# Performance work log

Hardware: AMD Instinct MI355X
Metric: run time of the kernel (lower is better)

Reference implementation:

```python
import jax, jax.numpy as jnp
import numpy as np

N_HEADS = 32
N_KV_HEADS = 8
HEAD_DIM = 128  # hidden 4096 / 32
NEG_INF = -1e9


def _apply_rope(x, cos, sin):
    # x: [B, S, H, D]; cos/sin: [S, D//2] -> complex multiply on (even, odd) pairs
    B, S, H, D = x.shape
    xr = x.reshape(B, S, H, D // 2, 2)
    a, b = xr[..., 0], xr[..., 1]
    c = cos[None, :, None, :]
    s = sin[None, :, None, :]
    out = jnp.stack([a * c - b * s, a * s + b * c], axis=-1)
    return out.reshape(B, S, H, D)


def setup_inputs() -> dict:
    key = jax.random.key(0)
    ks = jax.random.split(key, 8)
    B, S, HID = 1, 2048, 4096
    hidden_states = jax.random.normal(ks[0], (B, S, HID), dtype=jnp.float32)
    # causal additive mask [1,1,S,S]
    causal = jnp.tril(jnp.ones((S, S), dtype=bool))
    attention_mask = jnp.where(causal, 0.0, NEG_INF).astype(jnp.float32)[None, None]
    # true rotary frequencies (theta=500000 as in llama3)
    half = HEAD_DIM // 2
    inv_freq = 1.0 / (500000.0 ** (np.arange(0, half, dtype=np.float32) / half))
    angles = np.arange(S, dtype=np.float32)[:, None] * inv_freq[None, :]
    freqs_cos = jnp.asarray(np.cos(angles), dtype=jnp.float32)
    freqs_sin = jnp.asarray(np.sin(angles), dtype=jnp.float32)
    sc = 0.02
    wq = jax.random.normal(ks[1], (HID, HID), dtype=jnp.float32) * sc
    wk = jax.random.normal(ks[2], (N_KV_HEADS * HEAD_DIM, HID), dtype=jnp.float32) * sc
    wv = jax.random.normal(ks[3], (N_KV_HEADS * HEAD_DIM, HID), dtype=jnp.float32) * sc
    wo = jax.random.normal(ks[4], (HID, HID), dtype=jnp.float32) * sc
    return {"hidden_states": hidden_states, "attention_mask": attention_mask,
            "freqs_cos": freqs_cos, "freqs_sin": freqs_sin,
            "wq": wq, "wk": wk, "wv": wv, "wo": wo}


def reference(hidden_states, attention_mask, freqs_cos, freqs_sin, wq, wk, wv, wo):
    B, S, HID = hidden_states.shape
    n_rep = N_HEADS // N_KV_HEADS
    # projections (torch Linear: x @ W.T)
    q = (hidden_states @ wq.T).reshape(B, S, N_HEADS, HEAD_DIM)
    k = (hidden_states @ wk.T).reshape(B, S, N_KV_HEADS, HEAD_DIM)
    v = (hidden_states @ wv.T).reshape(B, S, N_KV_HEADS, HEAD_DIM)
    # rotary on q (full cos/sin) and k
    q = _apply_rope(q, freqs_cos, freqs_sin)
    k = _apply_rope(k, freqs_cos, freqs_sin)
    # [B, H, S, D]
    q = q.transpose(0, 2, 1, 3)
    k = k.transpose(0, 2, 1, 3)
    v = v.transpose(0, 2, 1, 3)
    # GQA: repeat_interleave kv heads
    k = jnp.repeat(k, n_rep, axis=1)
    v = jnp.repeat(v, n_rep, axis=1)
    scores = jnp.einsum("bhqd,bhkd->bhqk", q, k) / jnp.sqrt(jnp.float32(HEAD_DIM))
    scores = scores + attention_mask
    probs = jax.nn.softmax(scores.astype(jnp.float32), axis=-1)
    attn = jnp.einsum("bhqk,bhkd->bhqd", probs, v)
    attn = attn.transpose(0, 2, 1, 3).reshape(B, S, N_HEADS * HEAD_DIM)
    return attn @ wo.T
```

## Files before the change

### kernel.cpp

```cpp
#include <hip/hip_runtime.h>
#include <hip/hip_bf16.h>
#include <math.h>

#define SEQ 2048
#define HID 4096
#define NH 32
#define NKV 8
#define HD 128
#define KVG (NH / NKV)
#define NQKV 6144

typedef __bf16 bf16x8 __attribute__((ext_vector_type(8)));
typedef float  f32x4  __attribute__((ext_vector_type(4)));

__device__ __forceinline__ unsigned short f2bf(float f) {
  union { float f; unsigned int u; } v; v.f = f;
  unsigned int r = v.u + 0x7FFFu + ((v.u >> 16) & 1u);
  return (unsigned short)(r >> 16);
}
__device__ __forceinline__ float bf2f(unsigned short h) {
  union { unsigned int u; float f; } v; v.u = ((unsigned int)h) << 16;
  return v.f;
}

__device__ __forceinline__ void glds16(const unsigned short* g, unsigned short* l) {
  __builtin_amdgcn_global_load_lds(
      (const __attribute__((address_space(1))) void*)g,
      (__attribute__((address_space(3))) void*)l, 16, 0, 0);
}

#define MFMA_BF16 __builtin_amdgcn_mfma_f32_16x16x32_bf16

__global__ __launch_bounds__(256) void cvt_all(
    const float* __restrict__ H, const float* __restrict__ wq,
    const float* __restrict__ wk, const float* __restrict__ wv,
    const float* __restrict__ wo, unsigned short* __restrict__ ws)
{
  const long G1 = 1l << 20;
  const long M1 = 1l << 20;
  long g = (long)blockIdx.x * 256 + threadIdx.x;
  const float* src; unsigned short* dst; long rel;
  if      (g < 2 * G1) { src = H;  dst = ws;           rel = g;          }
  else if (g < 6 * G1) { src = wq; dst = ws + 8 * M1;  rel = g - 2 * G1; }
  else if (g < 7 * G1) { src = wk; dst = ws + 24 * M1; rel = g - 6 * G1; }
  else if (g < 8 * G1) { src = wv; dst = ws + 28 * M1; rel = g - 7 * G1; }
  else                 { src = wo; dst = ws + 32 * M1; rel = g - 8 * G1; }
  float4 v = ((const float4*)src)[rel];
  ushort4 o;
  o.x = f2bf(v.x); o.y = f2bf(v.y); o.z = f2bf(v.z); o.w = f2bf(v.w);
  ((ushort4*)dst)[rel] = o;
}

template<bool F32OUT>
__global__ __launch_bounds__(256) void gemm_nt(
    const unsigned short* __restrict__ A,
    const unsigned short* __restrict__ B,
    void* __restrict__ Cv,
    int M, int N, int K)
{
  __shared__ unsigned short As[128 * 64];
  __shared__ unsigned short Bs[128 * 64];
  const int t = threadIdx.x;
  const int lane = t & 63, wid = t >> 6;
  const int quad = lane >> 4, l16 = lane & 15;
  const int wm = (wid & 1) * 64, wn = (wid >> 1) * 64;
  const int m0 = blockIdx.y * 128, n0 = blockIdx.x * 128;

  int srow[4], sgch[4];
  const unsigned short* ga[4];
  const unsigned short* gb[4];
  unsigned short* la[4];
  unsigned short* lb[4];
  #pragma unroll
  for (int j = 0; j < 4; j++) {
    int pj = (wid * 4 + j) * 64 + lane;
    srow[j] = pj >> 3;
    sgch[j] = (pj & 7) ^ (srow[j] & 7);
    ga[j] = A + (size_t)(m0 + srow[j]) * K + sgch[j] * 8;
    gb[j] = B + (size_t)(n0 + srow[j]) * K + sgch[j] * 8;
    la[j] = &As[(wid * 4 + j) * 512];
    lb[j] = &Bs[(wid * 4 + j) * 512];
  }

  const f32x4 fzero = {0.f, 0.f, 0.f, 0.f};
  f32x4 acc[4][4];
  #pragma unroll
  for (int i = 0; i < 4; i++)
    #pragma unroll
    for (int j = 0; j < 4; j++) acc[i][j] = fzero;

  for (int k0 = 0; k0 < K; k0 += 64) {
    __syncthreads();
    #pragma unroll
    for (int j = 0; j < 4; j++) {
      glds16(ga[j], la[j]);
      glds16(gb[j], lb[j]);
      ga[j] += 64; gb[j] += 64;
    }
    __syncthreads();

    #pragma unroll
    for (int ks = 0; ks < 2; ks++) {
      bf16x8 af[4], bfr[4];
      #pragma unroll
      for (int mt = 0; mt < 4; mt++) {
        int row = wm + mt * 16 + l16;
        int cp = (ks * 4 + quad) ^ (l16 & 7);
        af[mt] = *(const bf16x8*)(&As[(row * 8 + cp) * 8]);
      }
      #pragma unroll
      for (int nt = 0; nt < 4; nt++) {
        int row = wn + nt * 16 + l16;
        int cp = (ks * 4 + quad) ^ (l16 & 7);
        bfr[nt] = *(const bf16x8*)(&Bs[(row * 8 + cp) * 8]);
      }
      #pragma unroll
      for (int mt = 0; mt < 4; mt++)
        #pragma unroll
        for (int nt = 0; nt < 4; nt++)
          acc[mt][nt] = MFMA_BF16(af[mt], bfr[nt], acc[mt][nt], 0, 0, 0);
    }
  }

  #pragma unroll
  for (int mt = 0; mt < 4; mt++)
    #pragma unroll
    for (int nt = 0; nt < 4; nt++)
      #pragma unroll
      for (int r = 0; r < 4; r++) {
        int row = m0 + wm + mt * 16 + quad * 4 + r;
        int col = n0 + wn + nt * 16 + l16;
        float v = acc[mt][nt][r];
        if (F32OUT) ((float*)Cv)[(size_t)row * N + col] = v;
        else        ((unsigned short*)Cv)[(size_t)row * N + col] = f2bf(v);
      }
}

__global__ __launch_bounds__(256) void rope_vtrans(
    const unsigned short* __restrict__ QKVr,
    const float* __restrict__ cosT,
    const float* __restrict__ sinT,
    unsigned short* __restrict__ Qh,
    unsigned short* __restrict__ Kh,
    unsigned short* __restrict__ Vtg)
{
  __shared__ unsigned short T[64 * 66];
  int hh = blockIdx.y;
  int bx = blockIdx.x;
  int t = threadIdx.x;
  if (hh < NH + NKV) {
    int sub = t >> 6, d2 = t & 63;
    int s = bx * 4 + sub;
    float c = cosT[s * 64 + d2], sn = sinT[s * 64 + d2];
    if (hh < NH) {
      const unsigned short* src = QKVr + (size_t)s * NQKV + hh * HD;
      unsigned short* dst = Qh + ((size_t)hh * SEQ + s) * HD;
      float a = bf2f(src[2 * d2]), b = bf2f(src[2 * d2 + 1]);
      dst[2 * d2]     = f2bf(a * c - b * sn);
      dst[2 * d2 + 1] = f2bf(a * sn + b * c);
    } else {
      int h = hh - NH;
      const unsigned short* src = QKVr + (size_t)s * NQKV + HID + h * HD;
      unsigned short* dst = Kh + ((size_t)h * SEQ + s) * HD;
      float a = bf2f(src[2 * d2]), b = bf2f(src[2 * d2 + 1]);
      dst[2 * d2]     = f2bf(a * c - b * sn);
      dst[2 * d2 + 1] = f2bf(a * sn + b * c);
    }
  } else {
    int idx = bx >> 5;
    int kvh = idx >> 1, d0 = (idx & 1) * 64;
    int s0 = (bx & 31) * 64;
    int si = t >> 2, dchunk = t & 3;
    const unsigned short* src = QKVr + (size_t)(s0 + si) * NQKV + HID + NKV * HD + kvh * HD + d0 + dchunk * 16;
    uint4 a = *(const uint4*)src;
    uint4 b = *(const uint4*)(src + 8);
    unsigned int va[8] = {a.x, a.y, a.z, a.w, b.x, b.y, b.z, b.w};
    #pragma unroll
    for (int j = 0; j < 8; j++)
      *(unsigned int*)(&T[si * 66 + dchunk * 16 + j * 2]) = va[j];
    __syncthreads();
    int di = t >> 2, schunk = t & 3;
    unsigned short px[16];
    #pragma unroll
    for (int j = 0; j < 16; j++) px[j] = T[(schunk * 16 + j) * 66 + di];
    unsigned short* dst = Vtg + ((size_t)kvh * HD + d0 + di) * SEQ + s0 + schunk * 16;
    *(uint4*)dst = *(uint4*)px;
    *(uint4*)(dst + 8) = *(uint4*)(px + 8);
  }
}

__global__ __launch_bounds__(256) void flash_kernel(
    const unsigned short* __restrict__ Qh,
    const unsigned short* __restrict__ Kh,
    const unsigned short* __restrict__ Vtg,
    unsigned short* __restrict__ Obf)
{
  __shared__ unsigned short Ks[2][64 * 128];
  __shared__ unsigned short Vs[2][128 * 64];
  __shared__ unsigned short Ps[4][16 * 72];

  const int h = blockIdx.y;
  const int pairp = blockIdx.x;
  const int kvh = h / KVG;
  const int t = threadIdx.x;
  const int lane = t & 63, w = t >> 6;
  const int quad = lane >> 4, l16 = lane & 15;
  const float scale = 0.08838834764831845f;
  const float SHIFT = 8.0f;

  bf16x8 ones;
  #pragma unroll
  for (int j = 0; j < 8; j++) ones[j] = (__bf16)1.0f;

  int krow[4], kgch[4], vrow[4], vgch[4];
  #pragma unroll
  for (int j = 0; j < 4; j++) {
    int pj = (w * 4 + j) * 64 + lane;
    krow[j] = pj >> 4; kgch[j] = (pj & 15) ^ (krow[j] & 15);
    vrow[j] = pj >> 3; vgch[j] = (pj & 7) ^ (vrow[j] & 7);
  }

  const unsigned short* Kbase = Kh + (size_t)kvh * SEQ * HD;
  const unsigned short* Vbase = Vtg + (size_t)kvh * HD * SEQ;

  auto stage = [&](int buf, int kv0) {
    #pragma unroll
    for (int j = 0; j < 4; j++) {
      glds16(Kbase + (size_t)(kv0 + krow[j]) * HD + kgch[j] * 8,
             &Ks[buf][(w * 4 + j) * 512]);
      glds16(Vbase + (size_t)vrow[j] * SEQ + kv0 + vgch[j] * 8,
             &Vs[buf][(w * 4 + j) * 512]);
    }
  };

  unsigned short* Pw = Ps[w];
  const f32x4 fzero = {0.f, 0.f, 0.f, 0.f};

  #pragma unroll
  for (int pass = 0; pass < 2; pass++) {
    const int qt = pass ? (31 - pairp) : pairp;
    const int q0 = qt * 64;
    const int q = q0 + w * 16 + l16;

    bf16x8 aq[4];
    const unsigned short* Qp = Qh + ((size_t)h * SEQ + q0 + w * 16 + l16) * HD;
    #pragma unroll
    for (int ks = 0; ks < 4; ks++) aq[ks] = *(const bf16x8*)(Qp + ks * 32 + quad * 8);

    f32x4 o[8];
    #pragma unroll
    for (int dt = 0; dt < 8; dt++) o[dt] = fzero;
    f32x4 lacc = fzero;

    const int nIt = (q0 >> 6) + 1;
    stage(0, 0);

    for (int it = 0; it < nIt; it++) {
      const int buf = it & 1;
      const int kv0 = it << 6;
      if (it + 1 < nIt) {
        stage(buf ^ 1, kv0 + 64);
        asm volatile("s_waitcnt vmcnt(8)" ::: "memory");
      } else {
        asm volatile("s_waitcnt vmcnt(0)" ::: "memory");
      }
      __builtin_amdgcn_s_barrier();

      const unsigned short* Kb = Ks[buf];
      const unsigned short* Vb = Vs[buf];

      f32x4 sc[4];
      #pragma unroll
      for (int kvt = 0; kvt < 4; kvt++) sc[kvt] = fzero;
      __builtin_amdgcn_s_setprio(1);
      #pragma unroll
      for (int ks = 0; ks < 4; ks++)
        #pragma unroll
        for (int kvt = 0; kvt < 4; kvt++) {
          int row = kvt * 16 + l16;
          int cp = (ks * 4 + quad) ^ l16;
          bf16x8 bk = *(const bf16x8*)(&Kb[(row * 16 + cp) * 8]);
          sc[kvt] = MFMA_BF16(bk, aq[ks], sc[kvt], 0, 0, 0);
        }
      __builtin_amdgcn_s_setprio(0);

      #pragma unroll
      for (int kvt = 0; kvt < 4; kvt++) {
        unsigned short ph[4];
        #pragma unroll
        for (int r = 0; r < 4; r++) {
          int kv = kv0 + kvt * 16 + quad * 4 + r;
          float p = (kv > q) ? 0.f : __expf(fmaf(sc[kvt][r], scale, -SHIFT));
          ph[r] = f2bf(p);
        }
        *(uint2*)(&Pw[l16 * 72 + kvt * 16 + quad * 4]) = *(const uint2*)ph;
      }

      __builtin_amdgcn_s_setprio(1);
      #pragma unroll
      for (int ks2 = 0; ks2 < 2; ks2++) {
        bf16x8 ap = *(const bf16x8*)(&Pw[l16 * 72 + ks2 * 32 + quad * 8]);
        lacc = MFMA_BF16(ap, ones, lacc, 0, 0, 0);
        #pragma unroll
        for (int dt = 0; dt < 8; dt++) {
          int row = dt * 16 + l16;
          int cp = (ks2 * 4 + quad) ^ (l16 & 7);
          bf16x8 bv = *(const bf16x8*)(&Vb[(row * 8 + cp) * 8]);
          o[dt] = MFMA_BF16(ap, bv, o[dt], 0, 0, 0);
        }
      }
      __builtin_amdgcn_s_setprio(0);
      __builtin_amdgcn_s_barrier();
    }

    #pragma unroll
    for (int dt = 0; dt < 8; dt++)
      #pragma unroll
      for (int r = 0; r < 4; r++) {
        int qq = q0 + w * 16 + quad * 4 + r;
        int d = dt * 16 + l16;
        Obf[(size_t)qq * HID + h * HD + d] = f2bf(o[dt][r] / lacc[r]);
      }
  }
}

extern "C" void kernel_launch(void* const* d_in, const int* in_sizes, int n_in,
                              void* d_out, int out_size, void* d_ws, size_t ws_size,
                              hipStream_t stream) {
  const float* H    = (const float*)d_in[0];
  const float* cosT = (const float*)d_in[2];
  const float* sinT = (const float*)d_in[3];
  const float* wq   = (const float*)d_in[4];
  const float* wk   = (const float*)d_in[5];
  const float* wv   = (const float*)d_in[6];
  const float* wo   = (const float*)d_in[7];

  unsigned short* ws = (unsigned short*)d_ws;
  const size_t M1 = 1u << 20;
  unsigned short* Hb   = ws;
  unsigned short* Wqkv = ws + (size_t)8  * M1;
  unsigned short* Wob  = ws + (size_t)32 * M1;
  unsigned short* QKVr = ws + (size_t)48 * M1;
  unsigned short* Qh   = ws + (size_t)8  * M1;
  unsigned short* Kh   = ws + (size_t)16 * M1;
  unsigned short* Vtg  = ws + (size_t)18 * M1;
  unsigned short* attn = ws;

  cvt_all<<<49152, 256, 0, stream>>>(H, wq, wk, wv, wo, ws);

  gemm_nt<false><<<dim3(48, 16), 256, 0, stream>>>(Hb, Wqkv, QKVr, SEQ, NQKV, HID);

  rope_vtrans<<<dim3(512, NH + NKV + 1), 256, 0, stream>>>(QKVr, cosT, sinT, Qh, Kh, Vtg);

  flash_kernel<<<dim3(16, NH), 256, 0, stream>>>(Qh, Kh, Vtg, attn);

  gemm_nt<true><<<dim3(32, 16), 256, 0, stream>>>(attn, Wob, d_out, SEQ, HID, HID);
}
```

Baseline: 482.5 us.

## Vectorize RoPE, split V transpose, grid-stride convert, skip mask off-diagonal

The fp32-to-bf16 convert kernel becomes a grid-stride loop over 2048 blocks instead of launching one thread per float4. RoPE for Q/K moves to its own kernel, where each thread handles 8 elements with 16-byte loads and stores and vectorized cos/sin reads, and the V transpose gets a separate launch. In flash attention the causal mask compare now runs only on diagonal tiles. Together these cut scalar memory traffic, launch overhead and per-element branching, at the cost of one extra kernel launch.

```diff
diff --git a/kernel.cpp b/kernel.cpp
--- a/kernel.cpp
+++ b/kernel.cpp
@@ -38,17 +38,20 @@
 {
   const long G1 = 1l << 20;
   const long M1 = 1l << 20;
-  long g = (long)blockIdx.x * 256 + threadIdx.x;
-  const float* src; unsigned short* dst; long rel;
-  if      (g < 2 * G1) { src = H;  dst = ws;           rel = g;          }
-  else if (g < 6 * G1) { src = wq; dst = ws + 8 * M1;  rel = g - 2 * G1; }
-  else if (g < 7 * G1) { src = wk; dst = ws + 24 * M1; rel = g - 6 * G1; }
-  else if (g < 8 * G1) { src = wv; dst = ws + 28 * M1; rel = g - 7 * G1; }
-  else                 { src = wo; dst = ws + 32 * M1; rel = g - 8 * G1; }
-  float4 v = ((const float4*)src)[rel];
-  ushort4 o;
-  o.x = f2bf(v.x); o.y = f2bf(v.y); o.z = f2bf(v.z); o.w = f2bf(v.w);
-  ((ushort4*)dst)[rel] = o;
+  const long TOT = 12 * G1;
+  const long stride = (long)gridDim.x * 256;
+  for (long g = (long)blockIdx.x * 256 + threadIdx.x; g < TOT; g += stride) {
+    const float* src; unsigned short* dst; long rel;
+    if      (g < 2 * G1) { src = H;  dst = ws;           rel = g;          }
+    else if (g < 6 * G1) { src = wq; dst = ws + 8 * M1;  rel = g - 2 * G1; }
+    else if (g < 7 * G1) { src = wk; dst = ws + 24 * M1; rel = g - 6 * G1; }
+    else if (g < 8 * G1) { src = wv; dst = ws + 28 * M1; rel = g - 7 * G1; }
+    else                 { src = wo; dst = ws + 32 * M1; rel = g - 8 * G1; }
+    float4 v = ((const float4*)src)[rel];
+    ushort4 o;
+    o.x = f2bf(v.x); o.y = f2bf(v.y); o.z = f2bf(v.z); o.w = f2bf(v.w);
+    ((ushort4*)dst)[rel] = o;
+  }
 }
 
 template<bool F32OUT>
@@ -136,57 +139,71 @@
       }
 }
 
-__global__ __launch_bounds__(256) void rope_vtrans(
+__global__ __launch_bounds__(256) void rope_qk(
     const unsigned short* __restrict__ QKVr,
     const float* __restrict__ cosT,
     const float* __restrict__ sinT,
     unsigned short* __restrict__ Qh,
-    unsigned short* __restrict__ Kh,
+    unsigned short* __restrict__ Kh)
+{
+  const int hh = blockIdx.y;
+  const int c = blockIdx.x * 256 + threadIdx.x;
+  const int s = c >> 4, ch = c & 15;
+  const int d0 = ch * 8;
+
+  const unsigned short* src;
+  unsigned short* dst;
+  if (hh < NH) {
+    src = QKVr + (size_t)s * NQKV + hh * HD + d0;
+    dst = Qh + ((size_t)hh * SEQ + s) * HD + d0;
+  } else {
+    int h = hh - NH;
+    src = QKVr + (size_t)s * NQKV + HID + h * HD + d0;
+    dst = Kh + ((size_t)h * SEQ + s) * HD + d0;
+  }
+
+  float4 cv = *(const float4*)(cosT + s * 64 + (d0 >> 1));
+  float4 sv = *(const float4*)(sinT + s * 64 + (d0 >> 1));
+  float cs[4] = {cv.x, cv.y, cv.z, cv.w};
+  float sn[4] = {sv.x, sv.y, sv.z, sv.w};
+
+  union { uint4 v; unsigned short u[8]; } in, out;
+  in.v = *(const uint4*)src;
+  #pragma unroll
+  for (int j = 0; j < 4; j++) {
+    float a = bf2f(in.u[2 * j]), b = bf2f(in.u[2 * j + 1]);
+    out.u[2 * j]     = f2bf(a * cs[j] - b * sn[j]);
+    out.u[2 * j + 1] = f2bf(a * sn[j] + b * cs[j]);
+  }
+  *(uint4*)dst = out.v;
+}
+
+__global__ __launch_bounds__(256) void vtrans(
+    const unsigned short* __restrict__ QKVr,
     unsigned short* __restrict__ Vtg)
 {
   __shared__ unsigned short T[64 * 66];
-  int hh = blockIdx.y;
   int bx = blockIdx.x;
   int t = threadIdx.x;
-  if (hh < NH + NKV) {
-    int sub = t >> 6, d2 = t & 63;
-    int s = bx * 4 + sub;
-    float c = cosT[s * 64 + d2], sn = sinT[s * 64 + d2];
-    if (hh < NH) {
-      const unsigned short* src = QKVr + (size_t)s * NQKV + hh * HD;
-      unsigned short* dst = Qh + ((size_t)hh * SEQ + s) * HD;
-      float a = bf2f(src[2 * d2]), b = bf2f(src[2 * d2 + 1]);
-      dst[2 * d2]     = f2bf(a * c - b * sn);
-      dst[2 * d2 + 1] = f2bf(a * sn + b * c);
-    } else {
-      int h = hh - NH;
-      const unsigned short* src = QKVr + (size_t)s * NQKV + HID + h * HD;
-      unsigned short* dst = Kh + ((size_t)h * SEQ + s) * HD;
-      float a = bf2f(src[2 * d2]), b = bf2f(src[2 * d2 + 1]);
-      dst[2 * d2]     = f2bf(a * c - b * sn);
-      dst[2 * d2 + 1] = f2bf(a * sn + b * c);
-    }
-  } else {
-    int idx = bx >> 5;
-    int kvh = idx >> 1, d0 = (idx & 1) * 64;
-    int s0 = (bx & 31) * 64;
-    int si = t >> 2, dchunk = t & 3;
-    const unsigned short* src = QKVr + (size_t)(s0 + si) * NQKV + HID + NKV * HD + kvh * HD + d0 + dchunk * 16;
-    uint4 a = *(const uint4*)src;
-    uint4 b = *(const uint4*)(src + 8);
-    unsigned int va[8] = {a.x, a.y, a.z, a.w, b.x, b.y, b.z, b.w};
-    #pragma unroll
-    for (int j = 0; j < 8; j++)
-      *(unsigned int*)(&T[si * 66 + dchunk * 16 + j * 2]) = va[j];
-    __syncthreads();
-    int di = t >> 2, schunk = t & 3;
-    unsigned short px[16];
-    #pragma unroll
-    for (int j = 0; j < 16; j++) px[j] = T[(schunk * 16 + j) * 66 + di];
-    unsigned short* dst = Vtg + ((size_t)kvh * HD + d0 + di) * SEQ + s0 + schunk * 16;
-    *(uint4*)dst = *(uint4*)px;
-    *(uint4*)(dst + 8) = *(uint4*)(px + 8);
-  }
+  int idx = bx >> 5;
+  int kvh = idx >> 1, d0 = (idx & 1) * 64;
+  int s0 = (bx & 31) * 64;
+  int si = t >> 2, dchunk = t & 3;
+  const unsigned short* src = QKVr + (size_t)(s0 + si) * NQKV + HID + NKV * HD + kvh * HD + d0 + dchunk * 16;
+  uint4 a = *(const uint4*)src;
+  uint4 b = *(const uint4*)(src + 8);
+  unsigned int va[8] = {a.x, a.y, a.z, a.w, b.x, b.y, b.z, b.w};
+  #pragma unroll
+  for (int j = 0; j < 8; j++)
+    *(unsigned int*)(&T[si * 66 + dchunk * 16 + j * 2]) = va[j];
+  __syncthreads();
+  int di = t >> 2, schunk = t & 3;
+  unsigned short px[16];
+  #pragma unroll
+  for (int j = 0; j < 16; j++) px[j] = T[(schunk * 16 + j) * 66 + di];
+  unsigned short* dst = Vtg + ((size_t)kvh * HD + d0 + di) * SEQ + s0 + schunk * 16;
+  *(uint4*)dst = *(uint4*)px;
+  *(uint4*)(dst + 8) = *(uint4*)(px + 8);
 }
 
 __global__ __launch_bounds__(256) void flash_kernel(
@@ -284,16 +301,27 @@
         }
       __builtin_amdgcn_s_setprio(0);
 
-      #pragma unroll
-      for (int kvt = 0; kvt < 4; kvt++) {
-        unsigned short ph[4];
-        #pragma unroll
-        for (int r = 0; r < 4; r++) {
-          int kv = kv0 + kvt * 16 + quad * 4 + r;
-          float p = (kv > q) ? 0.f : __expf(fmaf(sc[kvt][r], scale, -SHIFT));
-          ph[r] = f2bf(p);
+      if (kv0 == q0) {
+        #pragma unroll
+        for (int kvt = 0; kvt < 4; kvt++) {
+          unsigned short ph[4];
+          #pragma unroll
+          for (int r = 0; r < 4; r++) {
+            int kv = kv0 + kvt * 16 + quad * 4 + r;
+            float p = (kv > q) ? 0.f : __expf(fmaf(sc[kvt][r], scale, -SHIFT));
+            ph[r] = f2bf(p);
+          }
+          *(uint2*)(&Pw[l16 * 72 + kvt * 16 + quad * 4]) = *(const uint2*)ph;
         }
-        *(uint2*)(&Pw[l16 * 72 + kvt * 16 + quad * 4]) = *(const uint2*)ph;
+      } else {
+        #pragma unroll
+        for (int kvt = 0; kvt < 4; kvt++) {
+          unsigned short ph[4];
+          #pragma unroll
+          for (int r = 0; r < 4; r++)
+            ph[r] = f2bf(__expf(fmaf(sc[kvt][r], scale, -SHIFT)));
+          *(uint2*)(&Pw[l16 * 72 + kvt * 16 + quad * 4]) = *(const uint2*)ph;
+        }
       }
 
       __builtin_amdgcn_s_setprio(1);
@@ -346,11 +374,12 @@
   unsigned short* Vtg  = ws + (size_t)18 * M1;
   unsigned short* attn = ws;
 
-  cvt_all<<<49152, 256, 0, stream>>>(H, wq, wk, wv, wo, ws);
+  cvt_all<<<2048, 256, 0, stream>>>(H, wq, wk, wv, wo, ws);
 
   gemm_nt<false><<<dim3(48, 16), 256, 0, stream>>>(Hb, Wqkv, QKVr, SEQ, NQKV, HID);
 
-  rope_vtrans<<<dim3(512, NH + NKV + 1), 256, 0, stream>>>(QKVr, cosT, sinT, Qh, Kh, Vtg);
+  rope_qk<<<dim3(128, NH + NKV), 256, 0, stream>>>(QKVr, cosT, sinT, Qh, Kh);
+  vtrans<<<512, 256, 0, stream>>>(QKVr, Vtg);
 
   flash_kernel<<<dim3(16, NH), 256, 0, stream>>>(Qh, Kh, Vtg, attn);
 
```

Measured after the change: 481.2 us. Within noise of the previous version (-0.3%).
